# Performance work log

Measured on AMD Instinct MI355X. Metric: run time of the kernel, lower is better.

Reference implementation:

```python
import jax, jax.numpy as jnp
import numpy as np

BETA = 0.25
B, D, H, W = 32, 64, 32, 32
K = 1024


def setup_inputs() -> dict:
    key = jax.random.key(0)
    k1, k2 = jax.random.split(key)
    z = jax.random.normal(k1, (B, D, H, W), dtype=jnp.float32)
    embedding = jax.random.normal(k2, (K, D), dtype=jnp.float32)
    return {"z": z, "embedding": embedding}


def reference(z, embedding):
    # NCHW -> NHWC, flatten to [N, D]
    zp = jnp.transpose(z, (0, 2, 3, 1))          # [B,H,W,D]
    zf = zp.reshape(-1, zp.shape[-1])            # [N,D]
    # squared-distance matrix: ||z||^2 + ||e||^2 - 2 z e^T  -> [N,K]
    d = (jnp.sum(zf * zf, axis=1, keepdims=True)
         + jnp.sum(embedding * embedding, axis=1)
         - 2.0 * (zf @ embedding.T))
    min_encoding_indices = jnp.argmin(d, axis=1)  # [N]
    z_q = embedding[min_encoding_indices].reshape(zp.shape)  # [B,H,W,D]
    # commitment / codebook losses
    e_latent_loss = jnp.mean((jax.lax.stop_gradient(z_q) - zp) ** 2)
    q_latent_loss = jnp.mean((z_q - jax.lax.stop_gradient(zp)) ** 2)
    loss = q_latent_loss + BETA * e_latent_loss
    # straight-through estimator
    z_q_st = zp + jax.lax.stop_gradient(z_q - zp)
    z_q_out = jnp.transpose(z_q_st, (0, 3, 1, 2))  # back to NCHW
    return (z_q_out, min_encoding_indices, loss)
```

## Files before the change

kernel.cpp:

```cpp
#include <hip/hip_runtime.h>


#define IDX_OFF 2097152
#define LOSS_OFF 2129920
#define BIGF 160.0f
#define RL 72
#define U32INF 0xFFFFFFFFu

typedef __attribute__((ext_vector_type(8))) short bf16x8;
typedef __attribute__((ext_vector_type(4))) float f32x4;

__device__ __align__(256) float g_ep[1024 * RL];
__device__ __align__(256) float g_enb[1024];
__device__ __align__(256) unsigned short g_bf[64 * 4 * 64 * 8];
__device__ float g_partial[512];

typedef const __attribute__((address_space(1))) void* gvp;
typedef __attribute__((address_space(3))) void* lvp;

__device__ __forceinline__ void gll16(const void* g, void* l) {
    __builtin_amdgcn_global_load_lds((gvp)g, (lvp)l, 16, 0, 0);
}

__device__ __forceinline__ unsigned int f2bf(float f) {
    unsigned int u = __float_as_uint(f);
    return (u + 0x7FFFu + ((u >> 16) & 1u)) >> 16;
}

__device__ __forceinline__ unsigned int min16u(unsigned int x) {
#pragma unroll
    for (int o = 1; o < 16; o <<= 1) {
        unsigned int y = __shfl_xor((int)x, o, 64);
        x = y < x ? y : x;
    }
    return x;
}

__global__ __launch_bounds__(256) void vq_prep(const float* __restrict__ e) {
    int lane = threadIdx.x & 63;
    int k    = blockIdx.x * 4 + (threadIdx.x >> 6);
    float v  = e[k * 64 + lane];
    float m2 = -2.0f * v;
    float s  = v * v;
#pragma unroll
    for (int o = 32; o; o >>= 1) s += __shfl_xor(s, o, 64);
    g_ep[(size_t)k * RL + lane] = m2;
    if (lane == 0) { g_ep[(size_t)k * RL + 64] = s + BIGF; g_enb[k] = s + BIGF; }
    unsigned hb = f2bf(m2);
    float    hf = __uint_as_float(hb << 16);
    unsigned lb = f2bf(m2 - hf);
    int g  = k >> 4, c = k & 15;
    int ch = lane >> 5, dc = lane & 31;
    int g4 = dc >> 3,  j = dc & 7;
    int l  = g4 * 16 + c;
    g_bf[(size_t)((g * 4 + ch) * 64 + l) * 8 + j]     = (unsigned short)hb;
    g_bf[(size_t)((g * 4 + 2 + ch) * 64 + l) * 8 + j] = (unsigned short)lb;
}

__global__ __launch_bounds__(256, 2) void vq_main(const float* __restrict__ z,
                                                  const float* __restrict__ e,
                                                  float* __restrict__ out) {
    __shared__ unsigned short bf[2][8 * 2048];
    __shared__ float enb[1024];
    __shared__ int   stop[64][3];
    __shared__ unsigned long long skey[3][64];
    __shared__ int   ishare[64];
    __shared__ float lred[4];

    const int t    = threadIdx.x;
    const int lane = t & 63;
    const int w    = __builtin_amdgcn_readfirstlane(t >> 6);
    const int col  = lane & 15;
    const int g4   = lane >> 4;
    const int bid  = blockIdx.x;
    const int b    = bid >> 4;
    const int hw0  = (bid & 15) << 6;

    gll16((const char*)g_enb + w * 1024 + lane * 16, (char*)enb + w * 1024);
#pragma unroll
    for (int i = 0; i < 8; ++i) {
        int seg = w * 8 + i;
        gll16((const char*)g_bf + seg * 1024 + lane * 16, (char*)&bf[0][0] + seg * 1024);
    }

    const float* zr = z + (size_t)b * 65536 + hw0 + (w * 16 + col);
    bf16x8 zh[2], zl[2];
#pragma unroll
    for (int c = 0; c < 2; ++c)
#pragma unroll
        for (int j = 0; j < 8; ++j) {
            int d = c * 32 + g4 * 8 + j;
            float f = zr[(size_t)d * 1024];
            unsigned hb = f2bf(f);
            float    hf = __uint_as_float(hb << 16);
            unsigned lb = f2bf(f - hf);
            zh[c][j] = (short)hb;
            zl[c][j] = (short)lb;
        }

    unsigned int t0[4], t1[4], t2[4];
#pragma unroll
    for (int r = 0; r < 4; ++r) { t0[r] = U32INF; t1[r] = U32INF; t2[r] = U32INF; }

    __syncthreads();

    for (int tt = 0; tt < 8; ++tt) {
        const int cur = tt & 1;
        if (tt < 7) {
#pragma unroll
            for (int i = 0; i < 8; ++i) {
                int seg = w * 8 + i;
                gll16((const char*)g_bf + (tt + 1) * 32768 + seg * 1024 + lane * 16,
                      (char*)&bf[cur ^ 1][0] + seg * 1024);
            }
        }

        const unsigned short* bfc = &bf[cur][0];
#pragma unroll
        for (int gg = 0; gg < 8; ++gg) {
            const int kc = (tt * 8 + gg) * 16 + col;
            const bf16x8* p = (const bf16x8*)(bfc + gg * 2048);
            bf16x8 eh0 = p[0 * 64 + lane];
            bf16x8 eh1 = p[1 * 64 + lane];
            bf16x8 el0 = p[2 * 64 + lane];
            bf16x8 el1 = p[3 * 64 + lane];

            f32x4 acc = {0.f, 0.f, 0.f, 0.f};
            acc = __builtin_amdgcn_mfma_f32_16x16x32_bf16(zh[0], eh0, acc, 0, 0, 0);
            acc = __builtin_amdgcn_mfma_f32_16x16x32_bf16(zh[1], eh1, acc, 0, 0, 0);
            acc = __builtin_amdgcn_mfma_f32_16x16x32_bf16(zh[0], el0, acc, 0, 0, 0);
            acc = __builtin_amdgcn_mfma_f32_16x16x32_bf16(zh[1], el1, acc, 0, 0, 0);
            acc = __builtin_amdgcn_mfma_f32_16x16x32_bf16(zl[0], eh0, acc, 0, 0, 0);
            acc = __builtin_amdgcn_mfma_f32_16x16x32_bf16(zl[1], eh1, acc, 0, 0, 0);

            float enbv = enb[kc];
#pragma unroll
            for (int r = 0; r < 4; ++r) {
                float cand = acc[r] + enbv;
                unsigned int key = (__float_as_uint(cand) & 0xFFFFFC00u) | (unsigned)kc;
                unsigned int a0 = t0[r] < key ? t0[r] : key;
                unsigned int x  = t0[r] < key ? key : t0[r];
                unsigned int a1 = t1[r] < x ? t1[r] : x;
                unsigned int y  = t1[r] < x ? x : t1[r];
                unsigned int a2 = t2[r] < y ? t2[r] : y;
                t0[r] = a0; t1[r] = a1; t2[r] = a2;
            }
        }
        __syncthreads();
    }

#pragma unroll
    for (int r = 0; r < 4; ++r) {
        unsigned int x = t0[r], y = t1[r], zz = t2[r];
        unsigned int m1 = min16u(x);
        if (x == m1) { x = y; y = zz; zz = U32INF; }
        unsigned int m2 = min16u(x);
        if (x == m2) { x = y; }
        unsigned int m3 = min16u(x);
        int row = w * 16 + g4 * 4 + r;
        if (col == 0) {
            stop[row][0] = (int)(m1 & 1023u);
            stop[row][1] = (int)(m2 & 1023u);
            stop[row][2] = (int)(m3 & 1023u);
        }
    }
    __syncthreads();

    if (w < 3) {
        int kc = stop[lane][w];
        const float* zbase = z + (size_t)b * 65536 + hw0 + lane;
        const float* ep    = g_ep + (size_t)kc * RL;
        float d0 = 0.f, d1 = 0.f, d2 = 0.f, d3 = 0.f;
#pragma unroll
        for (int dq = 0; dq < 16; ++dq) {
            float4 ev = *(const float4*)(ep + dq * 4);
            d0 = fmaf(zbase[(size_t)(dq * 4 + 0) * 1024], ev.x, d0);
            d1 = fmaf(zbase[(size_t)(dq * 4 + 1) * 1024], ev.y, d1);
            d2 = fmaf(zbase[(size_t)(dq * 4 + 2) * 1024], ev.z, d2);
            d3 = fmaf(zbase[(size_t)(dq * 4 + 3) * 1024], ev.w, d3);
        }
        float dist = (d0 + d1) + (d2 + d3) + ep[64];
        skey[w][lane] = ((unsigned long long)__float_as_uint(dist) << 32) | (unsigned)kc;
    }
    __syncthreads();

    if (w == 0) {
        unsigned long long ky = skey[0][lane];
        unsigned long long k1 = skey[1][lane];
        unsigned long long k2 = skey[2][lane];
        ky = k1 < ky ? k1 : ky;
        ky = k2 < ky ? k2 : ky;
        int idx = (int)(ky & 0xFFFFFFFFull);
        out[IDX_OFF + bid * 64 + lane] = (float)idx;
        ishare[lane] = idx;
    }
    __syncthreads();

    {
        int idx = ishare[lane];
        const float*  zbase = z + (size_t)b * 65536 + hw0 + lane;
        float*        qbase = out + (size_t)b * 65536 + hw0 + lane;
        const float4* er4   = (const float4*)(e + (size_t)idx * 64) + (w << 2);

        float lsum = 0.f;
#pragma unroll
        for (int p = 0; p < 4; ++p) {
            float4 ev = er4[p];
            int d = (w << 4) + (p << 2);
            float ezw[4] = {ev.x, ev.y, ev.z, ev.w};
#pragma unroll
            for (int qq = 0; qq < 4; ++qq) {
                float zv = zbase[(size_t)(d + qq) * 1024];
                float df = ezw[qq] - zv;
                lsum = fmaf(df, df, lsum);
                qbase[(size_t)(d + qq) * 1024] = ezw[qq];
            }
        }
#pragma unroll
        for (int o = 32; o; o >>= 1) lsum += __shfl_xor(lsum, o, 64);
        if (lane == 0) lred[w] = lsum;
    }
    __syncthreads();
    if (t == 0)
        g_partial[bid] = (lred[0] + lred[1]) + (lred[2] + lred[3]);
}

__global__ __launch_bounds__(64) void vq_finish(float* __restrict__ out) {
    int lane = threadIdx.x;
    float s = 0.f;
#pragma unroll
    for (int i = 0; i < 8; ++i) s += g_partial[lane * 8 + i];
#pragma unroll
    for (int o = 32; o; o >>= 1) s += __shfl_xor(s, o, 64);
    if (lane == 0) out[LOSS_OFF] = s * (1.25f / 2097152.0f);
}

extern "C" void kernel_launch(void* const* d_in, const int* in_sizes, int n_in,
                              void* d_out, int out_size, void* d_ws, size_t ws_size,
                              hipStream_t stream) {
    const float* z = (const float*)d_in[0];
    const float* e = (const float*)d_in[1];
    float* out = (float*)d_out;

    vq_prep<<<256, 256, 0, stream>>>(e);
    vq_main<<<512, 256, 0, stream>>>(z, e, out);
    vq_finish<<<1, 64, 0, stream>>>(out);
}
```

Baseline: 34.21 us.

## Split codebook across warps with half-size row tiles and top-2 candidates

Each block now handles 32 spatial rows instead of 64, and the four warps form a 2x2 grid of row halves by codebook halves. The grid doubles to 1024 blocks and occupancy is raised to 4 blocks per CU. The per-lane candidate list shrinks from top-3 to top-2, and the MFMA chain is split into three independent accumulators to shorten dependency stalls. In return, each warp re-verifies fewer candidates in fp32, which slightly raises the risk of a wrong argmin, and more blocks each reload the codebook.

```diff
diff --git a/kernel.cpp b/kernel.cpp
--- a/kernel.cpp
+++ b/kernel.cpp
@@ -6,6 +6,7 @@
 #define BIGF 160.0f
 #define RL 72
 #define U32INF 0xFFFFFFFFu
+#define U64INF 0xFFFFFFFFFFFFFFFFull
 
 typedef __attribute__((ext_vector_type(8))) short bf16x8;
 typedef __attribute__((ext_vector_type(4))) float f32x4;
@@ -13,7 +14,7 @@
 __device__ __align__(256) float g_ep[1024 * RL];
 __device__ __align__(256) float g_enb[1024];
 __device__ __align__(256) unsigned short g_bf[64 * 4 * 64 * 8];
-__device__ float g_partial[512];
+__device__ float g_partial[1024];
 
 typedef const __attribute__((address_space(1))) void* gvp;
 typedef __attribute__((address_space(3))) void* lvp;
@@ -27,10 +28,10 @@
     return (u + 0x7FFFu + ((u >> 16) & 1u)) >> 16;
 }
 
-__device__ __forceinline__ unsigned int min16u(unsigned int x) {
+__device__ __forceinline__ unsigned long long min16u64(unsigned long long x) {
 #pragma unroll
     for (int o = 1; o < 16; o <<= 1) {
-        unsigned int y = __shfl_xor((int)x, o, 64);
+        unsigned long long y = __shfl_xor(x, o, 64);
         x = y < x ? y : x;
     }
     return x;
@@ -57,14 +58,14 @@
     g_bf[(size_t)((g * 4 + 2 + ch) * 64 + l) * 8 + j] = (unsigned short)lb;
 }
 
-__global__ __launch_bounds__(256, 2) void vq_main(const float* __restrict__ z,
+__global__ __launch_bounds__(256, 4) void vq_main(const float* __restrict__ z,
                                                   const float* __restrict__ e,
                                                   float* __restrict__ out) {
-    __shared__ unsigned short bf[2][8 * 2048];
+    __shared__ unsigned short bf[2][8192];
     __shared__ float enb[1024];
-    __shared__ int   stop[64][3];
-    __shared__ unsigned long long skey[3][64];
-    __shared__ int   ishare[64];
+    __shared__ int   stop[2][32][2];
+    __shared__ unsigned long long skey[4][32];
+    __shared__ int   ishare[32];
     __shared__ float lred[4];
 
     const int t    = threadIdx.x;
@@ -72,18 +73,22 @@
     const int w    = __builtin_amdgcn_readfirstlane(t >> 6);
     const int col  = lane & 15;
     const int g4   = lane >> 4;
+    const int rh   = w & 1;
+    const int kh   = w >> 1;
     const int bid  = blockIdx.x;
-    const int b    = bid >> 4;
-    const int hw0  = (bid & 15) << 6;
+    const int b    = bid >> 5;
+    const int hw0  = (bid & 31) << 5;
 
     gll16((const char*)g_enb + w * 1024 + lane * 16, (char*)enb + w * 1024);
 #pragma unroll
-    for (int i = 0; i < 8; ++i) {
-        int seg = w * 8 + i;
-        gll16((const char*)g_bf + seg * 1024 + lane * 16, (char*)&bf[0][0] + seg * 1024);
-    }
-
-    const float* zr = z + (size_t)b * 65536 + hw0 + (w * 16 + col);
+    for (int i = 0; i < 4; ++i) {
+        int s  = w * 4 + i;
+        int h  = s >> 3, ig = (s >> 2) & 1, f = s & 3;
+        gll16((const char*)g_bf + (size_t)(((h * 32 + ig) * 4 + f) * 1024) + lane * 16,
+              (char*)&bf[0][0] + s * 1024 + lane * 16);
+    }
+
+    const float* zr = z + (size_t)b * 65536 + hw0 + (rh * 16 + col);
     bf16x8 zh[2], zl[2];
 #pragma unroll
     for (int c = 0; c < 2; ++c)
@@ -98,52 +103,55 @@
             zl[c][j] = (short)lb;
         }
 
-    unsigned int t0[4], t1[4], t2[4];
-#pragma unroll
-    for (int r = 0; r < 4; ++r) { t0[r] = U32INF; t1[r] = U32INF; t2[r] = U32INF; }
-
-    __syncthreads();
-
-    for (int tt = 0; tt < 8; ++tt) {
+    unsigned int t0[4], t1[4];
+#pragma unroll
+    for (int r = 0; r < 4; ++r) { t0[r] = U32INF; t1[r] = U32INF; }
+
+    __syncthreads();
+
+    for (int tt = 0; tt < 16; ++tt) {
         const int cur = tt & 1;
-        if (tt < 7) {
-#pragma unroll
-            for (int i = 0; i < 8; ++i) {
-                int seg = w * 8 + i;
-                gll16((const char*)g_bf + (tt + 1) * 32768 + seg * 1024 + lane * 16,
-                      (char*)&bf[cur ^ 1][0] + seg * 1024);
+        if (tt < 15) {
+#pragma unroll
+            for (int i = 0; i < 4; ++i) {
+                int s  = w * 4 + i;
+                int h  = s >> 3, ig = (s >> 2) & 1, f = s & 3;
+                gll16((const char*)g_bf +
+                          (size_t)(((h * 32 + (tt + 1) * 2 + ig) * 4 + f) * 1024) + lane * 16,
+                      (char*)&bf[cur ^ 1][0] + s * 1024 + lane * 16);
             }
         }
 
         const unsigned short* bfc = &bf[cur][0];
 #pragma unroll
-        for (int gg = 0; gg < 8; ++gg) {
-            const int kc = (tt * 8 + gg) * 16 + col;
-            const bf16x8* p = (const bf16x8*)(bfc + gg * 2048);
-            bf16x8 eh0 = p[0 * 64 + lane];
-            bf16x8 eh1 = p[1 * 64 + lane];
-            bf16x8 el0 = p[2 * 64 + lane];
-            bf16x8 el1 = p[3 * 64 + lane];
-
-            f32x4 acc = {0.f, 0.f, 0.f, 0.f};
-            acc = __builtin_amdgcn_mfma_f32_16x16x32_bf16(zh[0], eh0, acc, 0, 0, 0);
-            acc = __builtin_amdgcn_mfma_f32_16x16x32_bf16(zh[1], eh1, acc, 0, 0, 0);
-            acc = __builtin_amdgcn_mfma_f32_16x16x32_bf16(zh[0], el0, acc, 0, 0, 0);
-            acc = __builtin_amdgcn_mfma_f32_16x16x32_bf16(zh[1], el1, acc, 0, 0, 0);
-            acc = __builtin_amdgcn_mfma_f32_16x16x32_bf16(zl[0], eh0, acc, 0, 0, 0);
-            acc = __builtin_amdgcn_mfma_f32_16x16x32_bf16(zl[1], eh1, acc, 0, 0, 0);
+        for (int i = 0; i < 2; ++i) {
+            const int gl = tt * 2 + i;
+            const int kc = kh * 512 + gl * 16 + col;
+            const bf16x8* p = (const bf16x8*)bfc + (kh * 2 + i) * 256;
+            bf16x8 eh0 = p[lane];
+            bf16x8 eh1 = p[64 + lane];
+            bf16x8 el0 = p[128 + lane];
+            bf16x8 el1 = p[192 + lane];
+
+            f32x4 aa = {0.f, 0.f, 0.f, 0.f};
+            f32x4 ab = {0.f, 0.f, 0.f, 0.f};
+            f32x4 ac = {0.f, 0.f, 0.f, 0.f};
+            aa = __builtin_amdgcn_mfma_f32_16x16x32_bf16(zh[0], eh0, aa, 0, 0, 0);
+            ab = __builtin_amdgcn_mfma_f32_16x16x32_bf16(zh[0], el0, ab, 0, 0, 0);
+            ac = __builtin_amdgcn_mfma_f32_16x16x32_bf16(zl[0], eh0, ac, 0, 0, 0);
+            aa = __builtin_amdgcn_mfma_f32_16x16x32_bf16(zh[1], eh1, aa, 0, 0, 0);
+            ab = __builtin_amdgcn_mfma_f32_16x16x32_bf16(zh[1], el1, ab, 0, 0, 0);
+            ac = __builtin_amdgcn_mfma_f32_16x16x32_bf16(zl[1], eh1, ac, 0, 0, 0);
 
             float enbv = enb[kc];
 #pragma unroll
             for (int r = 0; r < 4; ++r) {
-                float cand = acc[r] + enbv;
-                unsigned int key = (__float_as_uint(cand) & 0xFFFFFC00u) | (unsigned)kc;
+                float cand = (aa[r] + ab[r]) + (ac[r] + enbv);
+                unsigned int key = (__float_as_uint(cand) & ~31u) | (unsigned)gl;
                 unsigned int a0 = t0[r] < key ? t0[r] : key;
                 unsigned int x  = t0[r] < key ? key : t0[r];
                 unsigned int a1 = t1[r] < x ? t1[r] : x;
-                unsigned int y  = t1[r] < x ? x : t1[r];
-                unsigned int a2 = t2[r] < y ? t2[r] : y;
-                t0[r] = a0; t1[r] = a1; t2[r] = a2;
+                t0[r] = a0; t1[r] = a1;
             }
         }
         __syncthreads();
@@ -151,23 +159,25 @@
 
 #pragma unroll
     for (int r = 0; r < 4; ++r) {
-        unsigned int x = t0[r], y = t1[r], zz = t2[r];
-        unsigned int m1 = min16u(x);
-        if (x == m1) { x = y; y = zz; zz = U32INF; }
-        unsigned int m2 = min16u(x);
-        if (x == m2) { x = y; }
-        unsigned int m3 = min16u(x);
-        int row = w * 16 + g4 * 4 + r;
+        unsigned long long ku0 =
+            ((unsigned long long)(t0[r] & ~31u) << 32) |
+            (unsigned)(kh * 512 + (int)(t0[r] & 31u) * 16 + col);
+        unsigned long long ku1 =
+            ((unsigned long long)(t1[r] & ~31u) << 32) |
+            (unsigned)(kh * 512 + (int)(t1[r] & 31u) * 16 + col);
+        unsigned long long m1 = min16u64(ku0);
+        if (ku0 == m1) ku0 = ku1;
+        unsigned long long m2 = min16u64(ku0);
+        int row = rh * 16 + g4 * 4 + r;
         if (col == 0) {
-            stop[row][0] = (int)(m1 & 1023u);
-            stop[row][1] = (int)(m2 & 1023u);
-            stop[row][2] = (int)(m3 & 1023u);
-        }
-    }
-    __syncthreads();
-
-    if (w < 3) {
-        int kc = stop[lane][w];
+            stop[kh][row][0] = (int)(m1 & 1023u);
+            stop[kh][row][1] = (int)(m2 & 1023u);
+        }
+    }
+    __syncthreads();
+
+    if (lane < 32) {
+        int kc = stop[w >> 1][lane][w & 1];
         const float* zbase = z + (size_t)b * 65536 + hw0 + lane;
         const float* ep    = g_ep + (size_t)kc * RL;
         float d0 = 0.f, d1 = 0.f, d2 = 0.f, d3 = 0.f;
@@ -184,29 +194,33 @@
     }
     __syncthreads();
 
-    if (w == 0) {
+    if (w == 0 && lane < 32) {
         unsigned long long ky = skey[0][lane];
         unsigned long long k1 = skey[1][lane];
         unsigned long long k2 = skey[2][lane];
+        unsigned long long k3 = skey[3][lane];
         ky = k1 < ky ? k1 : ky;
         ky = k2 < ky ? k2 : ky;
+        ky = k3 < ky ? k3 : ky;
         int idx = (int)(ky & 0xFFFFFFFFull);
-        out[IDX_OFF + bid * 64 + lane] = (float)idx;
+        out[IDX_OFF + bid * 32 + lane] = (float)idx;
         ishare[lane] = idx;
     }
     __syncthreads();
 
     {
-        int idx = ishare[lane];
-        const float*  zbase = z + (size_t)b * 65536 + hw0 + lane;
-        float*        qbase = out + (size_t)b * 65536 + hw0 + lane;
-        const float4* er4   = (const float4*)(e + (size_t)idx * 64) + (w << 2);
+        int r  = t & 31;
+        int dg = t >> 5;
+        int idx = ishare[r];
+        const float*  zbase = z + (size_t)b * 65536 + hw0 + r;
+        float*        qbase = out + (size_t)b * 65536 + hw0 + r;
+        const float4* er4   = (const float4*)(e + (size_t)idx * 64) + dg * 2;
 
         float lsum = 0.f;
 #pragma unroll
-        for (int p = 0; p < 4; ++p) {
+        for (int p = 0; p < 2; ++p) {
             float4 ev = er4[p];
-            int d = (w << 4) + (p << 2);
+            int d = dg * 8 + p * 4;
             float ezw[4] = {ev.x, ev.y, ev.z, ev.w};
 #pragma unroll
             for (int qq = 0; qq < 4; ++qq) {
@@ -229,7 +243,7 @@
     int lane = threadIdx.x;
     float s = 0.f;
 #pragma unroll
-    for (int i = 0; i < 8; ++i) s += g_partial[lane * 8 + i];
+    for (int i = 0; i < 16; ++i) s += g_partial[lane * 16 + i];
 #pragma unroll
     for (int o = 32; o; o >>= 1) s += __shfl_xor(s, o, 64);
     if (lane == 0) out[LOSS_OFF] = s * (1.25f / 2097152.0f);
@@ -243,6 +257,6 @@
     float* out = (float*)d_out;
 
     vq_prep<<<256, 256, 0, stream>>>(e);
-    vq_main<<<512, 256, 0, stream>>>(z, e, out);
+    vq_main<<<1024, 256, 0, stream>>>(z, e, out);
     vq_finish<<<1, 64, 0, stream>>>(out);
 }
```

Result: slower. 39.57 us (+15.7%).
